# Performance work log

Hardware: AMD Instinct MI355X
Metric: run time of the kernel (lower is better)

Reference implementation:

```python
import jax, jax.numpy as jnp
import numpy as np

BETA = 1.0
B, N, D = 2048, 131072, 256

def setup_inputs() -> dict:
    key = jax.random.key(0)
    k1, k2 = jax.random.split(key)
    x = jax.random.normal(k1, (B, D), dtype=jnp.float32)
    stored = jax.random.normal(k2, (N, D), dtype=jnp.float32)
    return {"x": x, "stored": stored}

def reference(x, stored):
    # scores: [B, N] = beta * x @ stored^T
    scores = BETA * jnp.einsum('bd,nd->bn', x, stored)
    attn = jax.nn.softmax(scores, axis=-1)
    # retrieved patterns: [B, D]
    return jnp.einsum('bn,nd->bd', attn, stored)
```

## Files before the change

### kernel.cpp

```cpp
#include <hip/hip_runtime.h>
#include <hip/hip_bf16.h>
#include <math.h>

#define B_Q 2048
#define N_K 131072
#define D_DIM 256
#define NCHUNK 32
#define CHUNK_KEYS (N_K / NCHUNK)
#define KTILE 32
#define NITER (CHUNK_KEYS / KTILE)
#define NTILES (N_K / KTILE)
#define TILE_USHORTS 16384

typedef __attribute__((ext_vector_type(8))) _Float16 half8;
typedef __attribute__((ext_vector_type(8))) short bf16x8;
typedef __attribute__((ext_vector_type(2))) __fp16 fp16x2;
typedef __attribute__((ext_vector_type(4))) float f32x4;

static __device__ __forceinline__ unsigned pkrtz(float a, float b) {
    fp16x2 h = __builtin_amdgcn_cvt_pkrtz(a, b);
    return __builtin_bit_cast(unsigned, h);
}
static __device__ __forceinline__ unsigned short f2bf(float f) {
    unsigned u = __builtin_bit_cast(unsigned, f);
    unsigned r = (u + 0x7fffu + ((u >> 16) & 1u)) >> 16;
    return (unsigned short)r;
}

typedef const __attribute__((address_space(1))) unsigned int* gas_p;
typedef __attribute__((address_space(3))) unsigned int* las_p;
static __device__ __forceinline__ void gl_lds16(const void* g, void* l) {
    __builtin_amdgcn_global_load_lds((gas_p)g, (las_p)l, 16, 0, 0);
}

__global__ __launch_bounds__(512) void prepass(const float* __restrict__ stored,
                                               unsigned short* __restrict__ frag) {
    __shared__ float sh[32][270];
    const int tid = threadIdx.x;
    const int t = blockIdx.x;
    const float* src = stored + (size_t)t * 32 * 256;
#pragma unroll
    for (int i = 0; i < 8; ++i) {
        int gi = i * 512 + tid;
        int row = gi >> 7, c2 = (gi & 127) << 1;
        *(float2*)&sh[row][c2] = *(const float2*)(src + row * 256 + c2);
    }
    __syncthreads();
    unsigned short* out = frag + (size_t)t * TILE_USHORTS;
#pragma unroll
    for (int i = 0; i < 2; ++i) {
        int ck = i * 512 + tid;
        int lane = ck & 63, col = lane & 15, quad = lane >> 4;
        int kg = ck >> 9, s = (ck >> 6) & 7;
        int key = kg * 16 + col, d0 = s * 32 + quad * 8;
        union { uint4 v; unsigned e[4]; } o;
#pragma unroll
        for (int j2 = 0; j2 < 4; ++j2) {
            float2 f = *(const float2*)&sh[key][d0 + j2 * 2];
            o.e[j2] = pkrtz(f.x, f.y);
        }
        *(uint4*)(out + ck * 8) = o.v;
    }
#pragma unroll
    for (int i = 0; i < 2; ++i) {
        int cv = i * 512 + tid;
        int lane = cv & 63, col = lane & 15, quad = lane >> 4;
        int dn = cv >> 6;
        int d = dn * 16 + col;
        union { uint4 v; unsigned e[4]; } o;
#pragma unroll
        for (int j2 = 0; j2 < 4; ++j2) {
            float v0 = sh[quad * 4 + j2][d];
            float v1 = sh[16 + quad * 4 + j2][d];
            o.e[j2] = (unsigned)f2bf(v0) | ((unsigned)f2bf(v1) << 16);
        }
        *(uint4*)(out + 8192 + cv * 8) = o.v;
    }
}

__global__ __launch_bounds__(256, 2)
void hopfield_main(const float* __restrict__ x,
                   const unsigned short* __restrict__ frag,
                   float* __restrict__ partO,
                   float* __restrict__ partl) {
    __shared__ __align__(16) unsigned short Kb[2][8192];
    __shared__ __align__(16) unsigned short Vb[2][8192];
    __shared__ __align__(16) unsigned short Pb[4][32][40];

    const int tid = threadIdx.x;
    const int wave = tid >> 6, lane = tid & 63;
    const int col = lane & 15, quad = lane >> 4;
    const int blk = blockIdx.x;
    const int chunk = blk & 31, qb = blk >> 5;
    const int q0w = qb * 128 + wave * 32;
    const unsigned short* fbase = frag + (size_t)chunk * NITER * TILE_USHORTS;

    half8 xf[2][8];
    float ss[2] = {0.f, 0.f};
#pragma unroll
    for (int qg = 0; qg < 2; ++qg) {
        const float* xr = x + (size_t)(q0w + qg * 16 + col) * 256;
#pragma unroll
        for (int s = 0; s < 8; ++s) {
            f32x4 a = *(const f32x4*)(xr + s * 32 + quad * 8);
            f32x4 b = *(const f32x4*)(xr + s * 32 + quad * 8 + 4);
            union { half8 v; _Float16 e[8]; } h;
#pragma unroll
            for (int j = 0; j < 4; ++j) {
                h.e[j] = (_Float16)a[j]; h.e[4 + j] = (_Float16)b[j];
                ss[qg] += a[j] * a[j] + b[j] * b[j];
            }
            xf[qg][s] = h.v;
        }
    }
#pragma unroll
    for (int qg = 0; qg < 2; ++qg) {
        ss[qg] += __shfl_xor(ss[qg], 16);
        ss[qg] += __shfl_xor(ss[qg], 32);
    }
    float M0q[2] = {4.9f * sqrtf(ss[0]), 4.9f * sqrtf(ss[1])};
    float M0v[2][4];
#pragma unroll
    for (int qg = 0; qg < 2; ++qg)
#pragma unroll
        for (int r = 0; r < 4; ++r)
            M0v[qg][r] = __shfl(M0q[qg], quad * 4 + r);

    f32x4 O[2][16];
#pragma unroll
    for (int qg = 0; qg < 2; ++qg)
#pragma unroll
        for (int dn = 0; dn < 16; ++dn) O[qg][dn] = (f32x4){0.f, 0.f, 0.f, 0.f};
    float lacc[2][4] = {{0.f, 0.f, 0.f, 0.f}, {0.f, 0.f, 0.f, 0.f}};
    bf16x8 pa[2];
    pa[0] = (bf16x8){0,0,0,0,0,0,0,0};
    pa[1] = (bf16x8){0,0,0,0,0,0,0,0};

#pragma unroll
    for (int j = 0; j < 4; ++j) {
        int off = (wave * 4 + j) * 512 + lane * 8;
        gl_lds16(fbase + off, &Kb[0][off]);
        gl_lds16(fbase + 8192 + off, &Vb[0][off]);
    }

#pragma unroll 1
    for (int it = 0; it < NITER; ++it) {
        if (it) {
            const unsigned short* V = Vb[(it + 1) & 1];
#pragma unroll
            for (int dn = 0; dn < 16; ++dn) {
                bf16x8 bv = *(const bf16x8*)(V + (dn * 64 + lane) * 8);
                O[0][dn] = __builtin_amdgcn_mfma_f32_16x16x32_bf16(pa[0], bv, O[0][dn], 0, 0, 0);
                O[1][dn] = __builtin_amdgcn_mfma_f32_16x16x32_bf16(pa[1], bv, O[1][dn], 0, 0, 0);
            }
        }
        __syncthreads();

        const int itn = (it + 1 < NITER) ? it + 1 : it;
        const unsigned short* nbase = fbase + (size_t)itn * TILE_USHORTS;
#pragma unroll
        for (int j = 0; j < 4; ++j) {
            int off = (wave * 4 + j) * 512 + lane * 8;
            gl_lds16(nbase + off, &Kb[itn & 1][off]);
            gl_lds16(nbase + 8192 + off, &Vb[itn & 1][off]);
        }

        const unsigned short* K = Kb[it & 1];
        f32x4 S[2][2];
#pragma unroll
        for (int qg = 0; qg < 2; ++qg)
#pragma unroll
            for (int kg = 0; kg < 2; ++kg) S[qg][kg] = (f32x4){0.f, 0.f, 0.f, 0.f};
#pragma unroll
        for (int s = 0; s < 8; ++s) {
            half8 b0 = *(const half8*)(K + ((0 * 8 + s) * 64 + lane) * 8);
            half8 b1 = *(const half8*)(K + ((1 * 8 + s) * 64 + lane) * 8);
            S[0][0] = __builtin_amdgcn_mfma_f32_16x16x32_f16(xf[0][s], b0, S[0][0], 0, 0, 0);
            S[1][0] = __builtin_amdgcn_mfma_f32_16x16x32_f16(xf[1][s], b0, S[1][0], 0, 0, 0);
            S[0][1] = __builtin_amdgcn_mfma_f32_16x16x32_f16(xf[0][s], b1, S[0][1], 0, 0, 0);
            S[1][1] = __builtin_amdgcn_mfma_f32_16x16x32_f16(xf[1][s], b1, S[1][1], 0, 0, 0);
        }

        unsigned short* Pw = &Pb[wave][0][0];
#pragma unroll
        for (int qg = 0; qg < 2; ++qg)
#pragma unroll
            for (int r = 0; r < 4; ++r) {
                float m0 = M0v[qg][r];
                float p0 = __expf(S[qg][0][r] - m0);
                float p1 = __expf(S[qg][1][r] - m0);
                lacc[qg][r] += p0 + p1;
                int row = qg * 16 + quad * 4 + r;
                unsigned pk = (unsigned)f2bf(p0) | ((unsigned)f2bf(p1) << 16);
                *(unsigned*)(Pw + row * 40 + 2 * col) = pk;
            }
        asm volatile("s_waitcnt lgkmcnt(0)" ::: "memory");
#pragma unroll
        for (int qg = 0; qg < 2; ++qg)
            pa[qg] = *(const bf16x8*)&Pb[wave][qg * 16 + col][quad * 8];
    }

    {
        const unsigned short* V = Vb[(NITER - 1) & 1];
#pragma unroll
        for (int dn = 0; dn < 16; ++dn) {
            bf16x8 bv = *(const bf16x8*)(V + (dn * 64 + lane) * 8);
            O[0][dn] = __builtin_amdgcn_mfma_f32_16x16x32_bf16(pa[0], bv, O[0][dn], 0, 0, 0);
            O[1][dn] = __builtin_amdgcn_mfma_f32_16x16x32_bf16(pa[1], bv, O[1][dn], 0, 0, 0);
        }
    }

#pragma unroll
    for (int qg = 0; qg < 2; ++qg)
#pragma unroll
        for (int r = 0; r < 4; ++r) {
            float v = lacc[qg][r];
            v += __shfl_xor(v, 1); v += __shfl_xor(v, 2);
            v += __shfl_xor(v, 4); v += __shfl_xor(v, 8);
            if (col == 0)
                partl[(size_t)chunk * B_Q + q0w + qg * 16 + quad * 4 + r] = v;
        }
#pragma unroll
    for (int qg = 0; qg < 2; ++qg)
#pragma unroll
        for (int dn = 0; dn < 16; ++dn)
#pragma unroll
            for (int r = 0; r < 4; ++r) {
                int q = q0w + qg * 16 + quad * 4 + r;
                partO[((size_t)chunk * B_Q + q) * 256 + dn * 16 + col] = O[qg][dn][r];
            }
}

__global__ void combine_kernel(const float* __restrict__ partO,
                               const float* __restrict__ partl,
                               float* __restrict__ out) {
    const int q = blockIdx.x;
    const int d = threadIdx.x;
    float L = 0.f;
#pragma unroll
    for (int c = 0; c < NCHUNK; ++c) L += partl[(size_t)c * B_Q + q];
    float acc = 0.f;
#pragma unroll
    for (int c = 0; c < NCHUNK; ++c)
        acc += partO[((size_t)c * B_Q + q) * 256 + d];
    out[(size_t)q * 256 + d] = acc / L;
}

extern "C" void kernel_launch(void* const* d_in, const int* in_sizes, int n_in,
                              void* d_out, int out_size, void* d_ws, size_t ws_size,
                              hipStream_t stream) {
    const float* x      = (const float*)d_in[0];
    const float* stored = (const float*)d_in[1];
    float* out = (float*)d_out;

    char* wsb = (char*)d_ws;
    unsigned short* frag = (unsigned short*)wsb;
    float* partO = (float*)(wsb + (size_t)134217728);
    float* partl = (float*)(wsb + (size_t)134217728 + 67108864);

    prepass<<<NTILES, 512, 0, stream>>>(stored, frag);
    hopfield_main<<<512, 256, 0, stream>>>(x, frag, partO, partl);
    combine_kernel<<<B_Q, 256, 0, stream>>>(partO, partl, out);
}
```

Baseline: 484.5 us.

## Switch to 32x32 MFMA with transposed scores and register-only P handoff

Reworks the main kernel to use 32x32x16 MFMA instructions for both the QK^T and PV products, computing S transposed so each lane holds one query column and the softmax probabilities stay in registers. The shared-memory staging buffer for P is replaced by packed bf16 conversion and permlane32 swaps. The prepass fragment layout changes to match the new operand shapes, and exp is computed via exp2 with a fused multiply-add. This aims to cut LDS round trips, instruction count and per-row shuffles, at the cost of a more intricate lane mapping that must match the new layouts exactly.

```diff
diff --git a/kernel.cpp b/kernel.cpp
--- a/kernel.cpp
+++ b/kernel.cpp
@@ -16,6 +16,7 @@
 typedef __attribute__((ext_vector_type(8))) short bf16x8;
 typedef __attribute__((ext_vector_type(2))) __fp16 fp16x2;
 typedef __attribute__((ext_vector_type(4))) float f32x4;
+typedef __attribute__((ext_vector_type(16))) float f32x16;
 
 static __device__ __forceinline__ unsigned pkrtz(float a, float b) {
     fp16x2 h = __builtin_amdgcn_cvt_pkrtz(a, b);
@@ -25,6 +26,11 @@
     unsigned u = __builtin_bit_cast(unsigned, f);
     unsigned r = (u + 0x7fffu + ((u >> 16) & 1u)) >> 16;
     return (unsigned short)r;
+}
+static __device__ __forceinline__ unsigned cvt_pk_bf16(float lo, float hi) {
+    unsigned d;
+    asm("v_cvt_pk_bf16_f32 %0, %1, %2" : "=v"(d) : "v"(lo), "v"(hi));
+    return d;
 }
 
 typedef const __attribute__((address_space(1))) unsigned int* gas_p;
@@ -50,9 +56,9 @@
 #pragma unroll
     for (int i = 0; i < 2; ++i) {
         int ck = i * 512 + tid;
-        int lane = ck & 63, col = lane & 15, quad = lane >> 4;
-        int kg = ck >> 9, s = (ck >> 6) & 7;
-        int key = kg * 16 + col, d0 = s * 32 + quad * 8;
+        int l = ck & 63, s = ck >> 6;
+        int key = l & 31, h = l >> 5;
+        int d0 = s * 16 + h * 8;
         union { uint4 v; unsigned e[4]; } o;
 #pragma unroll
         for (int j2 = 0; j2 < 4; ++j2) {
@@ -64,14 +70,16 @@
 #pragma unroll
     for (int i = 0; i < 2; ++i) {
         int cv = i * 512 + tid;
-        int lane = cv & 63, col = lane & 15, quad = lane >> 4;
-        int dn = cv >> 6;
-        int d = dn * 16 + col;
+        int l = cv & 63, blkv = cv >> 6;
+        int dn = blkv >> 1, ks = blkv & 1;
+        int colv = l & 31, h = l >> 5;
+        int d = dn * 32 + colv;
+        int k0 = ks * 16 + h * 8;
         union { uint4 v; unsigned e[4]; } o;
 #pragma unroll
         for (int j2 = 0; j2 < 4; ++j2) {
-            float v0 = sh[quad * 4 + j2][d];
-            float v1 = sh[16 + quad * 4 + j2][d];
+            float v0 = sh[k0 + j2 * 2][d];
+            float v1 = sh[k0 + j2 * 2 + 1][d];
             o.e[j2] = (unsigned)f2bf(v0) | ((unsigned)f2bf(v1) << 16);
         }
         *(uint4*)(out + 8192 + cv * 8) = o.v;
@@ -85,53 +93,42 @@
                    float* __restrict__ partl) {
     __shared__ __align__(16) unsigned short Kb[2][8192];
     __shared__ __align__(16) unsigned short Vb[2][8192];
-    __shared__ __align__(16) unsigned short Pb[4][32][40];
 
     const int tid = threadIdx.x;
     const int wave = tid >> 6, lane = tid & 63;
-    const int col = lane & 15, quad = lane >> 4;
+    const int col = lane & 31, hf = lane >> 5;
     const int blk = blockIdx.x;
     const int chunk = blk & 31, qb = blk >> 5;
     const int q0w = qb * 128 + wave * 32;
     const unsigned short* fbase = frag + (size_t)chunk * NITER * TILE_USHORTS;
 
-    half8 xf[2][8];
-    float ss[2] = {0.f, 0.f};
-#pragma unroll
-    for (int qg = 0; qg < 2; ++qg) {
-        const float* xr = x + (size_t)(q0w + qg * 16 + col) * 256;
-#pragma unroll
-        for (int s = 0; s < 8; ++s) {
-            f32x4 a = *(const f32x4*)(xr + s * 32 + quad * 8);
-            f32x4 b = *(const f32x4*)(xr + s * 32 + quad * 8 + 4);
+    half8 xf[16];
+    float ss = 0.f;
+    {
+        const float* xr = x + (size_t)(q0w + col) * 256 + hf * 8;
+#pragma unroll
+        for (int s = 0; s < 16; ++s) {
+            f32x4 a = *(const f32x4*)(xr + s * 16);
+            f32x4 b = *(const f32x4*)(xr + s * 16 + 4);
             union { half8 v; _Float16 e[8]; } h;
 #pragma unroll
             for (int j = 0; j < 4; ++j) {
                 h.e[j] = (_Float16)a[j]; h.e[4 + j] = (_Float16)b[j];
-                ss[qg] += a[j] * a[j] + b[j] * b[j];
+                ss += a[j] * a[j] + b[j] * b[j];
             }
-            xf[qg][s] = h.v;
-        }
-    }
-#pragma unroll
-    for (int qg = 0; qg < 2; ++qg) {
-        ss[qg] += __shfl_xor(ss[qg], 16);
-        ss[qg] += __shfl_xor(ss[qg], 32);
-    }
-    float M0q[2] = {4.9f * sqrtf(ss[0]), 4.9f * sqrtf(ss[1])};
-    float M0v[2][4];
-#pragma unroll
-    for (int qg = 0; qg < 2; ++qg)
-#pragma unroll
-        for (int r = 0; r < 4; ++r)
-            M0v[qg][r] = __shfl(M0q[qg], quad * 4 + r);
-
-    f32x4 O[2][16];
-#pragma unroll
-    for (int qg = 0; qg < 2; ++qg)
-#pragma unroll
-        for (int dn = 0; dn < 16; ++dn) O[qg][dn] = (f32x4){0.f, 0.f, 0.f, 0.f};
-    float lacc[2][4] = {{0.f, 0.f, 0.f, 0.f}, {0.f, 0.f, 0.f, 0.f}};
+            xf[s] = h.v;
+        }
+    }
+    ss += __shfl_xor(ss, 32);
+    const float M0 = 4.9f * sqrtf(ss);
+    const float M0L = M0 * 1.44269504f;
+
+    f32x16 O[8];
+    const f32x16 z16 = {0.f,0.f,0.f,0.f,0.f,0.f,0.f,0.f,
+                        0.f,0.f,0.f,0.f,0.f,0.f,0.f,0.f};
+#pragma unroll
+    for (int dn = 0; dn < 8; ++dn) O[dn] = z16;
+    float lacc = 0.f;
     bf16x8 pa[2];
     pa[0] = (bf16x8){0,0,0,0,0,0,0,0};
     pa[1] = (bf16x8){0,0,0,0,0,0,0,0};
@@ -148,10 +145,11 @@
         if (it) {
             const unsigned short* V = Vb[(it + 1) & 1];
 #pragma unroll
-            for (int dn = 0; dn < 16; ++dn) {
-                bf16x8 bv = *(const bf16x8*)(V + (dn * 64 + lane) * 8);
-                O[0][dn] = __builtin_amdgcn_mfma_f32_16x16x32_bf16(pa[0], bv, O[0][dn], 0, 0, 0);
-                O[1][dn] = __builtin_amdgcn_mfma_f32_16x16x32_bf16(pa[1], bv, O[1][dn], 0, 0, 0);
+            for (int dn = 0; dn < 8; ++dn) {
+                bf16x8 bv0 = *(const bf16x8*)(V + ((dn * 2 + 0) * 64 + lane) * 8);
+                bf16x8 bv1 = *(const bf16x8*)(V + ((dn * 2 + 1) * 64 + lane) * 8);
+                O[dn] = __builtin_amdgcn_mfma_f32_32x32x16_bf16(pa[0], bv0, O[dn], 0, 0, 0);
+                O[dn] = __builtin_amdgcn_mfma_f32_32x32x16_bf16(pa[1], bv1, O[dn], 0, 0, 0);
             }
         }
         __syncthreads();
@@ -166,69 +164,63 @@
         }
 
         const unsigned short* K = Kb[it & 1];
-        f32x4 S[2][2];
-#pragma unroll
-        for (int qg = 0; qg < 2; ++qg)
-#pragma unroll
-            for (int kg = 0; kg < 2; ++kg) S[qg][kg] = (f32x4){0.f, 0.f, 0.f, 0.f};
-#pragma unroll
-        for (int s = 0; s < 8; ++s) {
-            half8 b0 = *(const half8*)(K + ((0 * 8 + s) * 64 + lane) * 8);
-            half8 b1 = *(const half8*)(K + ((1 * 8 + s) * 64 + lane) * 8);
-            S[0][0] = __builtin_amdgcn_mfma_f32_16x16x32_f16(xf[0][s], b0, S[0][0], 0, 0, 0);
-            S[1][0] = __builtin_amdgcn_mfma_f32_16x16x32_f16(xf[1][s], b0, S[1][0], 0, 0, 0);
-            S[0][1] = __builtin_amdgcn_mfma_f32_16x16x32_f16(xf[0][s], b1, S[0][1], 0, 0, 0);
-            S[1][1] = __builtin_amdgcn_mfma_f32_16x16x32_f16(xf[1][s], b1, S[1][1], 0, 0, 0);
-        }
-
-        unsigned short* Pw = &Pb[wave][0][0];
-#pragma unroll
-        for (int qg = 0; qg < 2; ++qg)
-#pragma unroll
-            for (int r = 0; r < 4; ++r) {
-                float m0 = M0v[qg][r];
-                float p0 = __expf(S[qg][0][r] - m0);
-                float p1 = __expf(S[qg][1][r] - m0);
-                lacc[qg][r] += p0 + p1;
-                int row = qg * 16 + quad * 4 + r;
-                unsigned pk = (unsigned)f2bf(p0) | ((unsigned)f2bf(p1) << 16);
-                *(unsigned*)(Pw + row * 40 + 2 * col) = pk;
-            }
-        asm volatile("s_waitcnt lgkmcnt(0)" ::: "memory");
-#pragma unroll
-        for (int qg = 0; qg < 2; ++qg)
-            pa[qg] = *(const bf16x8*)&Pb[wave][qg * 16 + col][quad * 8];
+        f32x16 S = z16;
+#pragma unroll
+        for (int s = 0; s < 16; ++s) {
+            half8 af = *(const half8*)(K + (s * 64 + lane) * 8);
+            S = __builtin_amdgcn_mfma_f32_32x32x16_f16(af, xf[s], S, 0, 0, 0);
+        }
+
+        float p[16];
+#pragma unroll
+        for (int r = 0; r < 16; ++r)
+            p[r] = __builtin_amdgcn_exp2f(fmaf(S[r], 1.44269504f, -M0L));
+        float ps01 = (p[0] + p[1]) + (p[2] + p[3]);
+        float ps23 = (p[4] + p[5]) + (p[6] + p[7]);
+        float ps45 = (p[8] + p[9]) + (p[10] + p[11]);
+        float ps67 = (p[12] + p[13]) + (p[14] + p[15]);
+        lacc += (ps01 + ps23) + (ps45 + ps67);
+
+        unsigned w0 = cvt_pk_bf16(p[0],  p[1]);
+        unsigned w1 = cvt_pk_bf16(p[2],  p[3]);
+        unsigned w2 = cvt_pk_bf16(p[4],  p[5]);
+        unsigned w3 = cvt_pk_bf16(p[6],  p[7]);
+        unsigned w4 = cvt_pk_bf16(p[8],  p[9]);
+        unsigned w5 = cvt_pk_bf16(p[10], p[11]);
+        unsigned w6 = cvt_pk_bf16(p[12], p[13]);
+        unsigned w7 = cvt_pk_bf16(p[14], p[15]);
+        asm volatile("v_permlane32_swap_b32 %0, %1" : "+v"(w0), "+v"(w2));
+        asm volatile("v_permlane32_swap_b32 %0, %1" : "+v"(w1), "+v"(w3));
+        asm volatile("v_permlane32_swap_b32 %0, %1" : "+v"(w4), "+v"(w6));
+        asm volatile("v_permlane32_swap_b32 %0, %1" : "+v"(w5), "+v"(w7));
+        union { bf16x8 v; unsigned u[4]; } A0, A1;
+        A0.u[0] = w0; A0.u[1] = w1; A0.u[2] = w2; A0.u[3] = w3;
+        A1.u[0] = w4; A1.u[1] = w5; A1.u[2] = w6; A1.u[3] = w7;
+        pa[0] = A0.v; pa[1] = A1.v;
     }
 
     {
         const unsigned short* V = Vb[(NITER - 1) & 1];
 #pragma unroll
-        for (int dn = 0; dn < 16; ++dn) {
-            bf16x8 bv = *(const bf16x8*)(V + (dn * 64 + lane) * 8);
-            O[0][dn] = __builtin_amdgcn_mfma_f32_16x16x32_bf16(pa[0], bv, O[0][dn], 0, 0, 0);
-            O[1][dn] = __builtin_amdgcn_mfma_f32_16x16x32_bf16(pa[1], bv, O[1][dn], 0, 0, 0);
-        }
-    }
-
-#pragma unroll
-    for (int qg = 0; qg < 2; ++qg)
-#pragma unroll
-        for (int r = 0; r < 4; ++r) {
-            float v = lacc[qg][r];
-            v += __shfl_xor(v, 1); v += __shfl_xor(v, 2);
-            v += __shfl_xor(v, 4); v += __shfl_xor(v, 8);
-            if (col == 0)
-                partl[(size_t)chunk * B_Q + q0w + qg * 16 + quad * 4 + r] = v;
-        }
-#pragma unroll
-    for (int qg = 0; qg < 2; ++qg)
-#pragma unroll
-        for (int dn = 0; dn < 16; ++dn)
-#pragma unroll
-            for (int r = 0; r < 4; ++r) {
-                int q = q0w + qg * 16 + quad * 4 + r;
-                partO[((size_t)chunk * B_Q + q) * 256 + dn * 16 + col] = O[qg][dn][r];
-            }
+        for (int dn = 0; dn < 8; ++dn) {
+            bf16x8 bv0 = *(const bf16x8*)(V + ((dn * 2 + 0) * 64 + lane) * 8);
+            bf16x8 bv1 = *(const bf16x8*)(V + ((dn * 2 + 1) * 64 + lane) * 8);
+            O[dn] = __builtin_amdgcn_mfma_f32_32x32x16_bf16(pa[0], bv0, O[dn], 0, 0, 0);
+            O[dn] = __builtin_amdgcn_mfma_f32_32x32x16_bf16(pa[1], bv1, O[dn], 0, 0, 0);
+        }
+    }
+
+    lacc += __shfl_xor(lacc, 32);
+    if (lane < 32)
+        partl[(size_t)chunk * B_Q + q0w + lane] = lacc;
+
+#pragma unroll
+    for (int dn = 0; dn < 8; ++dn)
+#pragma unroll
+        for (int r = 0; r < 16; ++r) {
+            int qrow = (r & 3) + 8 * (r >> 2) + 4 * hf;
+            partO[((size_t)chunk * B_Q + q0w + qrow) * 256 + dn * 32 + col] = O[dn][r];
+        }
 }
 
 __global__ void combine_kernel(const float* __restrict__ partO,
```

Result: no change. 477.5 us (-1.4%).
